# Kernel optimization log

Measured on AMD Instinct MI355X. Metric: run time of the kernel, lower is better.

## Reference

```python
import jax, jax.numpy as jnp
import numpy as np

D_MODEL = 300   # hardcoded d_model1 in Matposer.__init__
VOCAB = 32000
B, L = 512, 512
OUT = 4


def sinusoidal_pe(length, d):
    # Standard 'Attention is All You Need' positional encoding used by the repo's PositionalEncoding.
    pos = jnp.arange(length, dtype=jnp.float32)[:, None]
    div = jnp.exp(jnp.arange(0, d, 2, dtype=jnp.float32) * (-np.log(10000.0) / d))
    pe = jnp.zeros((length, d), dtype=jnp.float32)
    pe = pe.at[:, 0::2].set(jnp.sin(pos * div))
    pe = pe.at[:, 1::2].set(jnp.cos(pos * div))
    return pe


def setup_inputs() -> dict:
    key = jax.random.key(0)
    k1, k2, k3, k4, k5, k6 = jax.random.split(key, 6)
    return {
        "x1": jax.random.randint(k1, (B, L), 0, VOCAB, dtype=jnp.int32),
        "x2": jax.random.randint(k2, (B, L), 0, VOCAB, dtype=jnp.int32),
        "emb1": jax.random.normal(k3, (VOCAB, D_MODEL), dtype=jnp.float32) * 0.02,
        "emb2": jax.random.normal(k4, (VOCAB, D_MODEL), dtype=jnp.float32) * 0.02,
        "w1": jax.random.normal(k5, (D_MODEL, D_MODEL), dtype=jnp.float32) / np.sqrt(D_MODEL),
        "b1": jnp.zeros((D_MODEL,), dtype=jnp.float32),
        "w2": jax.random.normal(k6, (OUT, D_MODEL), dtype=jnp.float32) / np.sqrt(D_MODEL),
        "b2": jnp.zeros((OUT,), dtype=jnp.float32),
    }


def reference(x1, x2, emb1, emb2, w1, b1, w2, b2):
    scale = jnp.sqrt(jnp.float32(D_MODEL))   # Embeddings multiplies by sqrt(d_model)
    pe = sinusoidal_pe(x1.shape[1], D_MODEL)  # [L, D]
    # Embed + positional encoding (dropout=0 / eval mode). [B, L, D]
    e1 = emb1[x1] * scale + pe
    e2 = emb2[x2] * scale + pe
    # encoded_sents = e2.permute(0,2,1) @ e1 -> [B, D, D]
    fmap = jnp.einsum('bld,ble->bde', e2, e1)
    # torch Tensor.diagonal() defaults to dim1=0, dim2=1 -> shape [D, min(B, D)]
    diag = jnp.diagonal(fmap, axis1=0, axis2=1)  # [D, D] since B >= D
    # class_fc: Linear(300,300) -> ReLU -> Linear(300,output_size); torch Linear: x @ W.T + b
    h = jax.nn.relu(diag @ w1.T + b1)
    logits = h @ w2.T + b2
    # nn.Softmax() on a 2D input -> softmax over dim=1
    return jax.nn.softmax(logits, axis=-1)
```

## Files before the change

kernel.cpp:

```cpp
#include <hip/hip_runtime.h>
#include <math.h>

#define D_MODEL 300
#define LSEQ    512
#define NBATCH  300
#define SPLIT   4
#define LCH     (LSEQ / SPLIT)
#define KCH     (D_MODEL / SPLIT)
#define SCALE   17.32050807568877f

__global__ void pe_kernel(float* __restrict__ pe) {
    int idx = blockIdx.x * blockDim.x + threadIdx.x;
    if (idx >= LSEQ * D_MODEL) return;
    int l = idx / D_MODEL;
    int e = idx - l * D_MODEL;
    int k = e >> 1;
    float dv = expf((float)(2 * k) * (-9.210340371976184f / 300.0f));
    float arg = (float)l * dv;
    pe[idx] = (e & 1) ? cosf(arg) : sinf(arg);
}

__global__ void s_kernel(const int* __restrict__ x2, const float* __restrict__ emb2,
                         const float* __restrict__ pe, float* __restrict__ S) {
    const int i = blockIdx.x;
    const int l = threadIdx.x;
    int idx2 = x2[i * LSEQ + l];
    S[i * LSEQ + l] = emb2[idx2 * D_MODEL + i] * SCALE + pe[l * D_MODEL + i];
}

__global__ void diag_gather_kernel(const int* __restrict__ x1, const float* __restrict__ emb1,
                                   const float* __restrict__ S, float* __restrict__ Dm) {
    __shared__ int   x1ch[LCH];
    __shared__ float sch[LCH];
    const int i   = blockIdx.x;
    const int sp  = blockIdx.y;
    const int tid = threadIdx.x;
    const int l0  = sp * LCH;

    if (tid < LCH) {
        x1ch[tid] = x1[i * LSEQ + l0 + tid];
        sch[tid]  = S[i * LSEQ + l0 + tid];
    }
    __syncthreads();

    if (tid < D_MODEL) {
        float acc = 0.0f;
        #pragma unroll 8
        for (int l = 0; l < LCH; ++l)
            acc = fmaf(sch[l], emb1[x1ch[l] * D_MODEL + tid], acc);
        atomicAdd(&Dm[i * D_MODEL + tid], acc * SCALE);
    }
}

__global__ void diag_pe_kernel(const float* __restrict__ S, const float* __restrict__ pe,
                               float* __restrict__ Dm) {
    __shared__ float sch[LCH];
    const int i   = blockIdx.x;
    const int sp  = blockIdx.y;
    const int tid = threadIdx.x;
    const int l0  = sp * LCH;

    if (tid < LCH) sch[tid] = S[i * LSEQ + l0 + tid];
    __syncthreads();

    if (tid < D_MODEL) {
        float acc = 0.0f;
        #pragma unroll 8
        for (int l = 0; l < LCH; ++l)
            acc = fmaf(sch[l], pe[(l0 + l) * D_MODEL + tid], acc);
        atomicAdd(&Dm[i * D_MODEL + tid], acc);
    }
}

__global__ void fc1_kernel(const float* __restrict__ w1, const float* __restrict__ Dm,
                           float* __restrict__ Hpre) {
    const int j   = blockIdx.x;
    const int sp  = blockIdx.y;
    const int tid = threadIdx.x;
    const int k0  = sp * KCH;
    if (tid >= D_MODEL) return;
    const float* w1row = w1 + j * D_MODEL + k0;
    float acc = 0.0f;
    #pragma unroll 5
    for (int k = 0; k < KCH; ++k)
        acc = fmaf(w1row[k], Dm[(k0 + k) * D_MODEL + tid], acc);
    atomicAdd(&Hpre[j * D_MODEL + tid], acc);
}

__global__ void fc2_softmax_kernel(const float* __restrict__ Hpre, const float* __restrict__ b1,
                                   const float* __restrict__ w2, const float* __restrict__ b2,
                                   float* __restrict__ out) {
    __shared__ float sm[4][4][64];
    const int tid   = threadIdx.x;
    const int e_loc = tid & 63;
    const int jc    = tid >> 6;
    const int e     = blockIdx.x * 64 + e_loc;

    float a0 = 0.f, a1 = 0.f, a2 = 0.f, a3 = 0.f;
    if (e < D_MODEL) {
        const int j0 = jc * KCH;
        #pragma unroll 5
        for (int j = j0; j < j0 + KCH; ++j) {
            float h = fmaxf(Hpre[j * D_MODEL + e] + b1[j], 0.0f);
            a0 = fmaf(h, w2[0 * D_MODEL + j], a0);
            a1 = fmaf(h, w2[1 * D_MODEL + j], a1);
            a2 = fmaf(h, w2[2 * D_MODEL + j], a2);
            a3 = fmaf(h, w2[3 * D_MODEL + j], a3);
        }
    }
    sm[jc][0][e_loc] = a0; sm[jc][1][e_loc] = a1;
    sm[jc][2][e_loc] = a2; sm[jc][3][e_loc] = a3;
    __syncthreads();

    if (jc == 0 && e < D_MODEL) {
        float l0 = b2[0] + sm[0][0][e_loc] + sm[1][0][e_loc] + sm[2][0][e_loc] + sm[3][0][e_loc];
        float l1 = b2[1] + sm[0][1][e_loc] + sm[1][1][e_loc] + sm[2][1][e_loc] + sm[3][1][e_loc];
        float l2 = b2[2] + sm[0][2][e_loc] + sm[1][2][e_loc] + sm[2][2][e_loc] + sm[3][2][e_loc];
        float l3 = b2[3] + sm[0][3][e_loc] + sm[1][3][e_loc] + sm[2][3][e_loc] + sm[3][3][e_loc];
        float m  = fmaxf(fmaxf(l0, l1), fmaxf(l2, l3));
        float x0 = expf(l0 - m), x1 = expf(l1 - m), x2 = expf(l2 - m), x3 = expf(l3 - m);
        float inv = 1.0f / (x0 + x1 + x2 + x3);
        out[e * 4 + 0] = x0 * inv;
        out[e * 4 + 1] = x1 * inv;
        out[e * 4 + 2] = x2 * inv;
        out[e * 4 + 3] = x3 * inv;
    }
}

extern "C" void kernel_launch(void* const* d_in, const int* in_sizes, int n_in,
                              void* d_out, int out_size, void* d_ws, size_t ws_size,
                              hipStream_t stream) {
    const int*   x1   = (const int*)d_in[0];
    const int*   x2   = (const int*)d_in[1];
    const float* emb1 = (const float*)d_in[2];
    const float* emb2 = (const float*)d_in[3];
    const float* w1   = (const float*)d_in[4];
    const float* b1   = (const float*)d_in[5];
    const float* w2   = (const float*)d_in[6];
    const float* b2   = (const float*)d_in[7];
    float* out = (float*)d_out;

    char* ws = (char*)d_ws;
    float* pe   = (float*)ws;
    float* S    = (float*)(ws + 614400);
    float* Dm   = (float*)(ws + 1228800);
    float* Hpre = (float*)(ws + 1228800 + 360000);

    hipMemsetAsync(Dm, 0, 2 * 360000, stream);

    pe_kernel<<<(LSEQ * D_MODEL + 255) / 256, 256, 0, stream>>>(pe);
    s_kernel<<<NBATCH, LSEQ, 0, stream>>>(x2, emb2, pe, S);
    diag_gather_kernel<<<dim3(NBATCH, SPLIT), 320, 0, stream>>>(x1, emb1, S, Dm);
    diag_pe_kernel<<<dim3(NBATCH, SPLIT), 320, 0, stream>>>(S, pe, Dm);
    fc1_kernel<<<dim3(D_MODEL, SPLIT), 320, 0, stream>>>(w1, Dm, Hpre);
    fc2_softmax_kernel<<<(D_MODEL + 63) / 64, 256, 0, stream>>>(Hpre, b1, w2, b2, out);
}
```

Before: 165.5 us.

## Fuse S computation and diagonal gather/PE passes into one kernel; block fc1 rows

Folds the S-vector computation, the emb1 gather pass and the positional-encoding pass into a single diag kernel, so each block builds its S chunk in shared memory and accumulates (emb1*scale+pe) in one loop with one atomic per output. This removes two kernel launches, the S round trip through global memory, and a second set of atomics on Dm. fc1 now computes two output rows per block to reuse each Dm load, halving its grid. The fused loop does more loads per iteration, which could raise per-thread latency.

```diff
diff --git a/kernel.cpp b/kernel.cpp
--- a/kernel.cpp
+++ b/kernel.cpp
@@ -7,6 +7,7 @@
 #define SPLIT   4
 #define LCH     (LSEQ / SPLIT)
 #define KCH     (D_MODEL / SPLIT)
+#define JPB     2
 #define SCALE   17.32050807568877f
 
 __global__ void pe_kernel(float* __restrict__ pe) {
@@ -20,16 +21,9 @@
     pe[idx] = (e & 1) ? cosf(arg) : sinf(arg);
 }
 
-__global__ void s_kernel(const int* __restrict__ x2, const float* __restrict__ emb2,
-                         const float* __restrict__ pe, float* __restrict__ S) {
-    const int i = blockIdx.x;
-    const int l = threadIdx.x;
-    int idx2 = x2[i * LSEQ + l];
-    S[i * LSEQ + l] = emb2[idx2 * D_MODEL + i] * SCALE + pe[l * D_MODEL + i];
-}
-
-__global__ void diag_gather_kernel(const int* __restrict__ x1, const float* __restrict__ emb1,
-                                   const float* __restrict__ S, float* __restrict__ Dm) {
+__global__ void diag_fused_kernel(const int* __restrict__ x1, const int* __restrict__ x2,
+                                  const float* __restrict__ emb1, const float* __restrict__ emb2,
+                                  const float* __restrict__ pe, float* __restrict__ Dm) {
     __shared__ int   x1ch[LCH];
     __shared__ float sch[LCH];
     const int i   = blockIdx.x;
@@ -38,53 +32,43 @@
     const int l0  = sp * LCH;
 
     if (tid < LCH) {
-        x1ch[tid] = x1[i * LSEQ + l0 + tid];
-        sch[tid]  = S[i * LSEQ + l0 + tid];
+        const int l = l0 + tid;
+        x1ch[tid] = x1[i * LSEQ + l];
+        int idx2  = x2[i * LSEQ + l];
+        sch[tid]  = emb2[idx2 * D_MODEL + i] * SCALE + pe[l * D_MODEL + i];
     }
     __syncthreads();
 
     if (tid < D_MODEL) {
         float acc = 0.0f;
         #pragma unroll 8
-        for (int l = 0; l < LCH; ++l)
-            acc = fmaf(sch[l], emb1[x1ch[l] * D_MODEL + tid], acc);
-        atomicAdd(&Dm[i * D_MODEL + tid], acc * SCALE);
-    }
-}
-
-__global__ void diag_pe_kernel(const float* __restrict__ S, const float* __restrict__ pe,
-                               float* __restrict__ Dm) {
-    __shared__ float sch[LCH];
-    const int i   = blockIdx.x;
-    const int sp  = blockIdx.y;
-    const int tid = threadIdx.x;
-    const int l0  = sp * LCH;
-
-    if (tid < LCH) sch[tid] = S[i * LSEQ + l0 + tid];
-    __syncthreads();
-
-    if (tid < D_MODEL) {
-        float acc = 0.0f;
-        #pragma unroll 8
-        for (int l = 0; l < LCH; ++l)
-            acc = fmaf(sch[l], pe[(l0 + l) * D_MODEL + tid], acc);
+        for (int l = 0; l < LCH; ++l) {
+            float e1v = fmaf(emb1[x1ch[l] * D_MODEL + tid], SCALE,
+                             pe[(l0 + l) * D_MODEL + tid]);
+            acc = fmaf(sch[l], e1v, acc);
+        }
         atomicAdd(&Dm[i * D_MODEL + tid], acc);
     }
 }
 
 __global__ void fc1_kernel(const float* __restrict__ w1, const float* __restrict__ Dm,
                            float* __restrict__ Hpre) {
-    const int j   = blockIdx.x;
+    const int j0  = blockIdx.x * JPB;
     const int sp  = blockIdx.y;
     const int tid = threadIdx.x;
     const int k0  = sp * KCH;
     if (tid >= D_MODEL) return;
-    const float* w1row = w1 + j * D_MODEL + k0;
-    float acc = 0.0f;
+    const float* w1r0 = w1 + (j0 + 0) * D_MODEL + k0;
+    const float* w1r1 = w1 + (j0 + 1) * D_MODEL + k0;
+    float acc0 = 0.0f, acc1 = 0.0f;
     #pragma unroll 5
-    for (int k = 0; k < KCH; ++k)
-        acc = fmaf(w1row[k], Dm[(k0 + k) * D_MODEL + tid], acc);
-    atomicAdd(&Hpre[j * D_MODEL + tid], acc);
+    for (int k = 0; k < KCH; ++k) {
+        float d = Dm[(k0 + k) * D_MODEL + tid];
+        acc0 = fmaf(w1r0[k], d, acc0);
+        acc1 = fmaf(w1r1[k], d, acc1);
+    }
+    atomicAdd(&Hpre[(j0 + 0) * D_MODEL + tid], acc0);
+    atomicAdd(&Hpre[(j0 + 1) * D_MODEL + tid], acc1);
 }
 
 __global__ void fc2_softmax_kernel(const float* __restrict__ Hpre, const float* __restrict__ b1,
@@ -142,16 +126,13 @@
 
     char* ws = (char*)d_ws;
     float* pe   = (float*)ws;
-    float* S    = (float*)(ws + 614400);
-    float* Dm   = (float*)(ws + 1228800);
-    float* Hpre = (float*)(ws + 1228800 + 360000);
+    float* Dm   = (float*)(ws + 614400);
+    float* Hpre = (float*)(ws + 974400);
 
-    hipMemsetAsync(Dm, 0, 2 * 360000, stream);
+    (void)hipMemsetAsync(Dm, 0, 2 * 360000, stream);
 
     pe_kernel<<<(LSEQ * D_MODEL + 255) / 256, 256, 0, stream>>>(pe);
-    s_kernel<<<NBATCH, LSEQ, 0, stream>>>(x2, emb2, pe, S);
-    diag_gather_kernel<<<dim3(NBATCH, SPLIT), 320, 0, stream>>>(x1, emb1, S, Dm);
-    diag_pe_kernel<<<dim3(NBATCH, SPLIT), 320, 0, stream>>>(S, pe, Dm);
-    fc1_kernel<<<dim3(D_MODEL, SPLIT), 320, 0, stream>>>(w1, Dm, Hpre);
+    diag_fused_kernel<<<dim3(NBATCH, SPLIT), 320, 0, stream>>>(x1, x2, emb1, emb2, pe, Dm);
+    fc1_kernel<<<dim3(D_MODEL / JPB, SPLIT), 320, 0, stream>>>(w1, Dm, Hpre);
     fc2_softmax_kernel<<<(D_MODEL + 63) / 64, 256, 0, stream>>>(Hpre, b1, w2, b2, out);
 }
```

Result: faster. 160.2 us (-3.2%).
